# Kernel optimization log

Hardware: AMD Instinct MI355X
Metric: run time of the kernel (lower is better)

## Reference

```python
import jax, jax.numpy as jnp
import numpy as np

B, C, P, T = 16, 128, 512, 32
H = 2
D = C // H  # 64
SCALE = D ** -0.5  # note: original scales by d^-0.5, NOT (d*t)^-0.5


def setup_inputs() -> dict:
    key = jax.random.key(0)
    kx, kw, kb = jax.random.split(key, 3)
    x = jax.random.normal(kx, (B, C, P, T), dtype=jnp.float32)
    # Conv2d(C, 3C, kernel=1) == per-pixel linear: W:[3C, C], b:[3C]
    W = jax.random.normal(kw, (3 * C, C), dtype=jnp.float32) * (C ** -0.5)
    b = jax.random.normal(kb, (3 * C,), dtype=jnp.float32) * 0.01
    return {"x": x, "W": W, "b": b}


def reference(x, W, b):
    # 1x1 conv -> pointwise channel mix
    qkv = jnp.einsum('bcpt,oc->bopt', x, W) + b[None, :, None, None]  # [B,3C,P,T]
    qkv = qkv.reshape(B, 3, H, D, P, T)
    q, k, v = qkv[:, 0], qkv[:, 1], qkv[:, 2]  # each [B,H,D,P,T]
    # flatten (d t) as feature dim, tokens along P
    q = q.transpose(0, 1, 3, 2, 4).reshape(B, H, P, D * T)
    k = k.transpose(0, 1, 3, 2, 4).reshape(B, H, P, D * T)
    v = v.transpose(0, 1, 3, 2, 4).reshape(B, H, P, D * T)
    dots = jnp.einsum('bhpe,bhqe->bhpq', q, k) * SCALE  # [B,H,P,P]
    attn = jax.nn.softmax(dots, axis=-1)
    out = jnp.einsum('bhpq,bhqe->bhpe', attn, v)  # [B,H,P,D*T]
    # b h p (d t) -> b (h d) p t
    out = out.reshape(B, H, P, D, T).transpose(0, 1, 3, 2, 4).reshape(B, C, P, T)
    return out
```

## Files before the change

kernel.cpp:

```cpp
#include <hip/hip_runtime.h>

#define BB 16
#define CC 128
#define PP 512
#define TT 32
#define HH 2
#define DD 64
#define EE 2048
#define NPIX 16384
#define SCALE 0.125f

typedef _Float16 f16_t;
typedef _Float16 f16x8_t __attribute__((ext_vector_type(8)));
typedef float    f32x4_t __attribute__((ext_vector_type(4)));

#define AS_GLOBAL __attribute__((address_space(1)))
#define AS_LDS    __attribute__((address_space(3)))

__device__ __forceinline__ void async_ld16(const void* g, void* l) {
    __builtin_amdgcn_global_load_lds((const AS_GLOBAL void*)g,
                                     (AS_LDS void*)l, 16, 0, 0);
}

__device__ __forceinline__ void gemm_lds_bt(const f16_t* __restrict__ A, int lda,
                                            const f16_t* __restrict__ Bt, int ldb,
                                            int K, int m0, int n0,
                                            f16_t* As, f16_t* Bs,
                                            f32x4_t acc[4][4])
{
    const int tid  = threadIdx.x;
    const int lane = tid & 63;
    const int wave = tid >> 6;
    const int wm = wave & 1, wn = wave >> 1;
    const int quad = lane >> 4, l16 = lane & 15;

    const f16_t* gA0 = A  + (size_t)(m0 + lane)      * lda + wave * 8;
    const f16_t* gA1 = A  + (size_t)(m0 + 64 + lane) * lda + wave * 8;
    const f16_t* gB0 = Bt + (size_t)(n0 + lane)      * ldb + wave * 8;
    const f16_t* gB1 = Bt + (size_t)(n0 + 64 + lane) * ldb + wave * 8;
    f16_t* lA0 = As + (size_t)(wave * 128)      * 8;
    f16_t* lA1 = As + (size_t)(wave * 128 + 64) * 8;
    f16_t* lB0 = Bs + (size_t)(wave * 128)      * 8;
    f16_t* lB1 = Bs + (size_t)(wave * 128 + 64) * 8;

    const int ar = wm * 64 + l16;
    const int br = wn * 64 + l16;

    for (int k0 = 0; k0 < K; k0 += 32) {
        if (k0) __syncthreads();
        async_ld16(gA0 + k0, lA0);
        async_ld16(gA1 + k0, lA1);
        async_ld16(gB0 + k0, lB0);
        async_ld16(gB1 + k0, lB1);
        __syncthreads();

        f16x8_t af[4], bf[4];
#pragma unroll
        for (int mi = 0; mi < 4; ++mi)
            af[mi] = *(const f16x8_t*)(As + (size_t)(quad * 128 + ar + mi * 16) * 8);
#pragma unroll
        for (int ni = 0; ni < 4; ++ni)
            bf[ni] = *(const f16x8_t*)(Bs + (size_t)(quad * 128 + br + ni * 16) * 8);
#pragma unroll
        for (int mi = 0; mi < 4; ++mi)
#pragma unroll
            for (int ni = 0; ni < 4; ++ni)
                acc[mi][ni] = __builtin_amdgcn_mfma_f32_16x16x32_f16(
                    af[mi], bf[ni], acc[mi][ni], 0, 0, 0);
    }
}

__global__ __launch_bounds__(256) void proj_kernel(const float* __restrict__ x,
                                                   const float* __restrict__ W,
                                                   const float* __restrict__ bias,
                                                   f16_t* __restrict__ q,
                                                   f16_t* __restrict__ k,
                                                   f16_t* __restrict__ v)
{
    __shared__ float xs[CC * 128];
    const int b    = blockIdx.y;
    const int s    = blockIdx.x >> 7;
    const int pt   = blockIdx.x & 127;
    const int tid  = threadIdx.x;
    const int lane = tid & 63;
    const int wave = tid >> 6;
    const int wm   = wave & 1, wn = wave >> 1;
    const int quad = lane >> 4, l16 = lane & 15;
    const int pixb = pt * 128;

    const float* xb = x + (size_t)b * CC * NPIX;

#pragma unroll
    for (int ii = 0; ii < 16; ++ii) {
        const int i = wave * 16 + ii;
        const float* g = xb + (size_t)(i * 2 + (lane >> 5)) * NPIX
                            + pixb + (lane & 31) * 4;
        async_ld16(g, xs + i * 256);
    }
    __syncthreads();

    f32x4_t acc[4][4];
#pragma unroll
    for (int i = 0; i < 4; ++i)
#pragma unroll
        for (int j = 0; j < 4; ++j) acc[i][j] = (f32x4_t){0.f, 0.f, 0.f, 0.f};

#pragma unroll
    for (int k0 = 0; k0 < CC; k0 += 32) {
        const int kq = k0 + quad * 8;
        f16x8_t af[4], bf[4];
#pragma unroll
        for (int mi = 0; mi < 4; ++mi) {
            const int o = s * 128 + wm * 64 + mi * 16 + l16;
            const float* wp = W + o * CC + kq;
            const float4 w0 = *(const float4*)wp;
            const float4 w1 = *(const float4*)(wp + 4);
            f16x8_t t;
            t[0] = (_Float16)w0.x; t[1] = (_Float16)w0.y;
            t[2] = (_Float16)w0.z; t[3] = (_Float16)w0.w;
            t[4] = (_Float16)w1.x; t[5] = (_Float16)w1.y;
            t[6] = (_Float16)w1.z; t[7] = (_Float16)w1.w;
            af[mi] = t;
        }
#pragma unroll
        for (int ni = 0; ni < 4; ++ni) {
            const int pl = wn * 64 + ni * 16 + l16;
            f16x8_t t;
#pragma unroll
            for (int j = 0; j < 8; ++j)
                t[j] = (_Float16)xs[(kq + j) * 128 + pl];
            bf[ni] = t;
        }
#pragma unroll
        for (int mi = 0; mi < 4; ++mi)
#pragma unroll
            for (int ni = 0; ni < 4; ++ni)
                acc[mi][ni] = __builtin_amdgcn_mfma_f32_16x16x32_f16(
                    af[mi], bf[ni], acc[mi][ni], 0, 0, 0);
    }

    f16_t* dst = (s == 0) ? q : (s == 1) ? k : v;
#pragma unroll
    for (int mi = 0; mi < 4; ++mi) {
#pragma unroll
        for (int r = 0; r < 4; ++r) {
            const int o_loc = wm * 64 + mi * 16 + quad * 4 + r;
            const int o     = s * 128 + o_loc;
            const float bv  = bias[o];
            const int h = o_loc >> 6, d = o_loc & 63;
#pragma unroll
            for (int ni = 0; ni < 4; ++ni) {
                const int pix = pixb + wn * 64 + ni * 16 + l16;
                const int p = pix >> 5, t = pix & 31;
                const size_t addr =
                    ((size_t)((b * HH + h) * PP + p)) * EE + d * TT + t;
                dst[addr] = (_Float16)(acc[mi][ni][r] + bv);
            }
        }
    }
}

__global__ __launch_bounds__(256) void vpose_kernel(const f16_t* __restrict__ v,
                                                    f16_t* __restrict__ vt)
{
    __shared__ unsigned short lds[64][65];
    const int bh   = blockIdx.y;
    const int tile = blockIdx.x;
    const int e0 = (tile & 31) * 64;
    const int p0 = (tile >> 5) * 64;
    const int tid = threadIdx.x;
    const int r0 = tid >> 6;
    const int cc = tid & 63;
    const f16_t* vb  = v  + (size_t)bh * PP * EE;
    f16_t*       vtb = vt + (size_t)bh * EE * PP;
#pragma unroll
    for (int it = 0; it < 16; ++it) {
        const int pl = it * 4 + r0;
        lds[pl][cc] = __builtin_bit_cast(unsigned short,
                          vb[(size_t)(p0 + pl) * EE + e0 + cc]);
    }
    __syncthreads();
#pragma unroll
    for (int it = 0; it < 16; ++it) {
        const int el = it * 4 + r0;
        vtb[(size_t)(e0 + el) * PP + p0 + cc] =
            __builtin_bit_cast(_Float16, lds[cc][el]);
    }
}

__global__ __launch_bounds__(256) void qk_kernel(const f16_t* __restrict__ q,
                                                 const f16_t* __restrict__ k,
                                                 float* __restrict__ S)
{
    __shared__ f16_t As[128 * 32];
    __shared__ f16_t Bs[128 * 32];
    const int id = blockIdx.x;
    const int bh = id & 31;
    const int tile = id >> 5;
    const int mt = tile & 3, nt = tile >> 2;
    const int tid  = threadIdx.x;
    const int lane = tid & 63;
    const int wave = tid >> 6;
    const int wm = wave & 1, wn = wave >> 1;
    const int quad = lane >> 4, l16 = lane & 15;

    f32x4_t acc[4][4];
#pragma unroll
    for (int i = 0; i < 4; ++i)
#pragma unroll
        for (int j = 0; j < 4; ++j) acc[i][j] = (f32x4_t){0.f, 0.f, 0.f, 0.f};

    const f16_t* qb = q + (size_t)bh * PP * EE;
    const f16_t* kb = k + (size_t)bh * PP * EE;
    gemm_lds_bt(qb, EE, kb, EE, EE, mt * 128, nt * 128, As, Bs, acc);

    float* Sb = S + (size_t)bh * PP * PP;
#pragma unroll
    for (int mi = 0; mi < 4; ++mi)
#pragma unroll
        for (int r = 0; r < 4; ++r) {
            const int row = mt * 128 + wm * 64 + mi * 16 + quad * 4 + r;
#pragma unroll
            for (int ni = 0; ni < 4; ++ni) {
                const int col = nt * 128 + wn * 64 + ni * 16 + l16;
                Sb[(size_t)row * PP + col] = acc[mi][ni][r] * SCALE;
            }
        }
}

__global__ __launch_bounds__(256) void softmax_kernel(float* __restrict__ S)
{
    const int tid  = threadIdx.x;
    const int wave = tid >> 6;
    const int lane = tid & 63;
    const int row  = blockIdx.x * 4 + wave;
    float* rp = S + (size_t)row * PP;

    const float4 a = *(const float4*)(rp + lane * 8);
    const float4 b = *(const float4*)(rp + lane * 8 + 4);

    float m = fmaxf(fmaxf(fmaxf(a.x, a.y), fmaxf(a.z, a.w)),
                    fmaxf(fmaxf(b.x, b.y), fmaxf(b.z, b.w)));
#pragma unroll
    for (int off = 1; off < 64; off <<= 1) m = fmaxf(m, __shfl_xor(m, off, 64));

    float e[8];
    e[0] = expf(a.x - m); e[1] = expf(a.y - m);
    e[2] = expf(a.z - m); e[3] = expf(a.w - m);
    e[4] = expf(b.x - m); e[5] = expf(b.y - m);
    e[6] = expf(b.z - m); e[7] = expf(b.w - m);

    float sum = e[0] + e[1] + e[2] + e[3] + e[4] + e[5] + e[6] + e[7];
#pragma unroll
    for (int off = 1; off < 64; off <<= 1) sum += __shfl_xor(sum, off, 64);
    const float inv = 1.0f / sum;

    __syncthreads();

    f16_t* prow = (f16_t*)rp;
    f16x8_t o;
#pragma unroll
    for (int j = 0; j < 8; ++j) o[j] = (_Float16)(e[j] * inv);
    *(f16x8_t*)(prow + lane * 8) = o;
}

__global__ __launch_bounds__(256) void pv_kernel(const f16_t* __restrict__ Pm,
                                                 const f16_t* __restrict__ vt,
                                                 float* __restrict__ out)
{
    __shared__ f16_t As[128 * 32];
    __shared__ f16_t Bs[128 * 32];
    const int id = blockIdx.x;
    const int bh = id & 31;
    const int tile = id >> 5;
    const int mt = tile & 3, nt = tile >> 2;
    const int tid  = threadIdx.x;
    const int lane = tid & 63;
    const int wave = tid >> 6;
    const int wm = wave & 1, wn = wave >> 1;
    const int quad = lane >> 4, l16 = lane & 15;

    f32x4_t acc[4][4];
#pragma unroll
    for (int i = 0; i < 4; ++i)
#pragma unroll
        for (int j = 0; j < 4; ++j) acc[i][j] = (f32x4_t){0.f, 0.f, 0.f, 0.f};

    const f16_t* Pb  = Pm + (size_t)bh * PP * 1024;
    const f16_t* vtb = vt + (size_t)bh * EE * PP;
    gemm_lds_bt(Pb, 1024, vtb, PP, PP, mt * 128, nt * 128, As, Bs, acc);

    const int b = bh >> 1, h = bh & 1;
#pragma unroll
    for (int mi = 0; mi < 4; ++mi)
#pragma unroll
        for (int r = 0; r < 4; ++r) {
            const int p = mt * 128 + wm * 64 + mi * 16 + quad * 4 + r;
#pragma unroll
            for (int ni = 0; ni < 4; ++ni) {
                const int e = nt * 128 + wn * 64 + ni * 16 + l16;
                const int d = e >> 5, t = e & 31;
                out[(((size_t)(b * CC + h * DD + d)) * PP + p) * TT + t] =
                    acc[mi][ni][r];
            }
        }
}

extern "C" void kernel_launch(void* const* d_in, const int* in_sizes, int n_in,
                              void* d_out, int out_size, void* d_ws, size_t ws_size,
                              hipStream_t stream)
{
    const float* x    = (const float*)d_in[0];
    const float* W    = (const float*)d_in[1];
    const float* bias = (const float*)d_in[2];
    float* out = (float*)d_out;

    char* ws = (char*)d_ws;
    const size_t MiB = 1024ull * 1024ull;
    f16_t* q  = (f16_t*)(ws);
    f16_t* k  = (f16_t*)(ws + 64 * MiB);
    f16_t* v  = (f16_t*)(ws + 128 * MiB);
    f16_t* vt = (f16_t*)(ws + 192 * MiB);
    float* S  = (float*)(ws + 256 * MiB);

    proj_kernel<<<dim3(384, 16), dim3(256), 0, stream>>>(x, W, bias, q, k, v);
    vpose_kernel<<<dim3(256, 32), dim3(256), 0, stream>>>(v, vt);
    qk_kernel<<<dim3(512), dim3(256), 0, stream>>>(q, k, S);
    softmax_kernel<<<dim3(4096), dim3(256), 0, stream>>>(S);
    pv_kernel<<<dim3(2048), dim3(256), 0, stream>>>((const f16_t*)S, vt, out);
}
```

Before: 541.4 us.

## Reuse one fp16 x tile for q, k and v projections; pre-convert W

The projection kernel now loads each 128-pixel x tile once, converts it to fp16 into a swizzled LDS layout, and loops over the three q/k/v output slices. Before, three separate blocks each reloaded the fp32 tile. A small extra kernel converts W to fp16 once, so the per-block float-to-half conversion of weights goes away. This cuts global reads of x by a factor of three and removes scalar LDS conversions, at the cost of fewer blocks (128x16 instead of 384x16) and synchronous global loads replacing async LDS loads. Wh reuses the S workspace region, which is only written later.

```diff
diff --git a/kernel.cpp b/kernel.cpp
--- a/kernel.cpp
+++ b/kernel.cpp
@@ -12,6 +12,7 @@
 
 typedef _Float16 f16_t;
 typedef _Float16 f16x8_t __attribute__((ext_vector_type(8)));
+typedef _Float16 f16x4_t __attribute__((ext_vector_type(4)));
 typedef float    f32x4_t __attribute__((ext_vector_type(4)));
 
 #define AS_GLOBAL __attribute__((address_space(1)))
@@ -70,17 +71,27 @@
     }
 }
 
+__global__ __launch_bounds__(256) void wcvt_kernel(const float* __restrict__ W,
+                                                   f16_t* __restrict__ Wh)
+{
+    const int i = (blockIdx.x * 256 + threadIdx.x) * 4;
+    const float4 wv = *(const float4*)(W + i);
+    f16x4_t t;
+    t[0] = (_Float16)wv.x; t[1] = (_Float16)wv.y;
+    t[2] = (_Float16)wv.z; t[3] = (_Float16)wv.w;
+    *(f16x4_t*)(Wh + i) = t;
+}
+
 __global__ __launch_bounds__(256) void proj_kernel(const float* __restrict__ x,
-                                                   const float* __restrict__ W,
+                                                   const f16_t* __restrict__ Wh,
                                                    const float* __restrict__ bias,
                                                    f16_t* __restrict__ q,
                                                    f16_t* __restrict__ k,
                                                    f16_t* __restrict__ v)
 {
-    __shared__ float xs[CC * 128];
+    __shared__ f16_t xs[CC * 128];
     const int b    = blockIdx.y;
-    const int s    = blockIdx.x >> 7;
-    const int pt   = blockIdx.x & 127;
+    const int pt   = blockIdx.x;
     const int tid  = threadIdx.x;
     const int lane = tid & 63;
     const int wave = tid >> 6;
@@ -90,71 +101,69 @@
 
     const float* xb = x + (size_t)b * CC * NPIX;
 
-#pragma unroll
-    for (int ii = 0; ii < 16; ++ii) {
-        const int i = wave * 16 + ii;
-        const float* g = xb + (size_t)(i * 2 + (lane >> 5)) * NPIX
-                            + pixb + (lane & 31) * 4;
-        async_ld16(g, xs + i * 256);
+#pragma unroll 2
+    for (int r = 0; r < 8; ++r) {
+        const int u  = r * 4 + wave;
+        const int c0 = (u >> 1) * 8;
+        const int pl = (u & 1) * 64 + lane;
+        const float* g = xb + (size_t)c0 * NPIX + pixb + pl;
+        float vv[8];
+#pragma unroll
+        for (int j = 0; j < 8; ++j) vv[j] = g[(size_t)j * NPIX];
+        f16x8_t t;
+#pragma unroll
+        for (int j = 0; j < 8; ++j) t[j] = (_Float16)vv[j];
+        *(f16x8_t*)((char*)xs + pl * 256 + ((c0 * 2) ^ ((pl & 15) << 4))) = t;
     }
     __syncthreads();
 
-    f32x4_t acc[4][4];
-#pragma unroll
-    for (int i = 0; i < 4; ++i)
-#pragma unroll
-        for (int j = 0; j < 4; ++j) acc[i][j] = (f32x4_t){0.f, 0.f, 0.f, 0.f};
-
-#pragma unroll
-    for (int k0 = 0; k0 < CC; k0 += 32) {
-        const int kq = k0 + quad * 8;
-        f16x8_t af[4], bf[4];
+    for (int s = 0; s < 3; ++s) {
+        f32x4_t acc[4][4];
+#pragma unroll
+        for (int i = 0; i < 4; ++i)
+#pragma unroll
+            for (int j = 0; j < 4; ++j) acc[i][j] = (f32x4_t){0.f, 0.f, 0.f, 0.f};
+
+#pragma unroll
+        for (int k0 = 0; k0 < CC; k0 += 32) {
+            const int kq = k0 + quad * 8;
+            f16x8_t af[4], bf[4];
+#pragma unroll
+            for (int mi = 0; mi < 4; ++mi) {
+                const int o = s * 128 + wm * 64 + mi * 16 + l16;
+                af[mi] = *(const f16x8_t*)(Wh + (size_t)o * CC + kq);
+            }
+#pragma unroll
+            for (int ni = 0; ni < 4; ++ni) {
+                const int pl = wn * 64 + ni * 16 + l16;
+                bf[ni] = *(const f16x8_t*)((char*)xs + pl * 256 +
+                                           ((kq * 2) ^ ((pl & 15) << 4)));
+            }
+#pragma unroll
+            for (int mi = 0; mi < 4; ++mi)
+#pragma unroll
+                for (int ni = 0; ni < 4; ++ni)
+                    acc[mi][ni] = __builtin_amdgcn_mfma_f32_16x16x32_f16(
+                        af[mi], bf[ni], acc[mi][ni], 0, 0, 0);
+        }
+
+        f16_t* dst = (s == 0) ? q : (s == 1) ? k : v;
 #pragma unroll
         for (int mi = 0; mi < 4; ++mi) {
-            const int o = s * 128 + wm * 64 + mi * 16 + l16;
-            const float* wp = W + o * CC + kq;
-            const float4 w0 = *(const float4*)wp;
-            const float4 w1 = *(const float4*)(wp + 4);
-            f16x8_t t;
-            t[0] = (_Float16)w0.x; t[1] = (_Float16)w0.y;
-            t[2] = (_Float16)w0.z; t[3] = (_Float16)w0.w;
-            t[4] = (_Float16)w1.x; t[5] = (_Float16)w1.y;
-            t[6] = (_Float16)w1.z; t[7] = (_Float16)w1.w;
-            af[mi] = t;
-        }
-#pragma unroll
-        for (int ni = 0; ni < 4; ++ni) {
-            const int pl = wn * 64 + ni * 16 + l16;
-            f16x8_t t;
-#pragma unroll
-            for (int j = 0; j < 8; ++j)
-                t[j] = (_Float16)xs[(kq + j) * 128 + pl];
-            bf[ni] = t;
-        }
-#pragma unroll
-        for (int mi = 0; mi < 4; ++mi)
-#pragma unroll
-            for (int ni = 0; ni < 4; ++ni)
-                acc[mi][ni] = __builtin_amdgcn_mfma_f32_16x16x32_f16(
-                    af[mi], bf[ni], acc[mi][ni], 0, 0, 0);
-    }
-
-    f16_t* dst = (s == 0) ? q : (s == 1) ? k : v;
-#pragma unroll
-    for (int mi = 0; mi < 4; ++mi) {
-#pragma unroll
-        for (int r = 0; r < 4; ++r) {
-            const int o_loc = wm * 64 + mi * 16 + quad * 4 + r;
-            const int o     = s * 128 + o_loc;
-            const float bv  = bias[o];
-            const int h = o_loc >> 6, d = o_loc & 63;
-#pragma unroll
-            for (int ni = 0; ni < 4; ++ni) {
-                const int pix = pixb + wn * 64 + ni * 16 + l16;
-                const int p = pix >> 5, t = pix & 31;
-                const size_t addr =
-                    ((size_t)((b * HH + h) * PP + p)) * EE + d * TT + t;
-                dst[addr] = (_Float16)(acc[mi][ni][r] + bv);
+#pragma unroll
+            for (int r = 0; r < 4; ++r) {
+                const int o_loc = wm * 64 + mi * 16 + quad * 4 + r;
+                const int o     = s * 128 + o_loc;
+                const float bv  = bias[o];
+                const int h = o_loc >> 6, d = o_loc & 63;
+#pragma unroll
+                for (int ni = 0; ni < 4; ++ni) {
+                    const int pix = pixb + wn * 64 + ni * 16 + l16;
+                    const int p = pix >> 5, t = pix & 31;
+                    const size_t addr =
+                        ((size_t)((b * HH + h) * PP + p)) * EE + d * TT + t;
+                    dst[addr] = (_Float16)(acc[mi][ni][r] + bv);
+                }
             }
         }
     }
@@ -322,8 +331,10 @@
     f16_t* v  = (f16_t*)(ws + 128 * MiB);
     f16_t* vt = (f16_t*)(ws + 192 * MiB);
     float* S  = (float*)(ws + 256 * MiB);
-
-    proj_kernel<<<dim3(384, 16), dim3(256), 0, stream>>>(x, W, bias, q, k, v);
+    f16_t* Wh = (f16_t*)(ws + 256 * MiB);
+
+    wcvt_kernel<<<dim3(48), dim3(256), 0, stream>>>(W, Wh);
+    proj_kernel<<<dim3(128, 16), dim3(256), 0, stream>>>(x, Wh, bias, q, k, v);
     vpose_kernel<<<dim3(256, 32), dim3(256), 0, stream>>>(v, vt);
     qk_kernel<<<dim3(512), dim3(256), 0, stream>>>(q, k, S);
     softmax_kernel<<<dim3(4096), dim3(256), 0, stream>>>(S);
```

Measured after the change: 510.2 us. 1.06x faster.
